# Kernel optimization log

Hardware: AMD Instinct MI355X
Metric: run time of the kernel (lower is better)

Reference implementation:

```python
import jax, jax.numpy as jnp
import numpy as np

G = 4        # split_group
H = 64       # hidden_size_t = 256 // 4 (causal -> //1)
I = 64       # input_size_t  = 256 // 4
EPS = 1e-5


def _lstm(x, W_ih, W_hh, b):
    """Grouped unidirectional LSTM, PyTorch gate order (i,f,g,o).
    x: (G,B,T,I); W_ih: (G,4H,I); W_hh: (G,4H,H); b: (G,4H) -> (G,B,T,H)"""
    g, bsz, t, _ = x.shape
    h_dim = W_hh.shape[-1]
    # precompute input projections for all timesteps
    xp = jnp.einsum('gbti,gki->gbtk', x, W_ih) + b[:, None, None, :]  # (G,B,T,4H)
    xp = jnp.moveaxis(xp, 2, 0)  # (T,G,B,4H)

    def step(carry, xt):
        h, c = carry
        gates = xt + jnp.einsum('gbh,gkh->gbk', h, W_hh)
        i_g, f_g, g_g, o_g = jnp.split(gates, 4, axis=-1)
        i_g = jax.nn.sigmoid(i_g)
        f_g = jax.nn.sigmoid(f_g)
        g_g = jnp.tanh(g_g)
        o_g = jax.nn.sigmoid(o_g)
        c = f_g * c + i_g * g_g
        h = o_g * jnp.tanh(c)
        return (h, c), h

    h0 = jnp.zeros((g, bsz, h_dim), x.dtype)
    _, hs = jax.lax.scan(step, (h0, h0), xp)  # hs: (T,G,B,H)
    return jnp.moveaxis(hs, 0, 2)  # (G,B,T,H)


def _bn(x, gamma, beta):
    """BatchNorm1d (training stats) over (B,T) per feature. x: (B,T,F)"""
    mean = x.mean(axis=(0, 1))
    var = x.var(axis=(0, 1))
    return (x - mean) * jax.lax.rsqrt(var + EPS) * gamma + beta


def setup_inputs() -> dict:
    key = jax.random.key(0)
    ks = jax.random.split(key, 12)
    s = 0.1
    F = G * H
    return {
        'inpt': jax.random.normal(ks[0], (32, 1000, 256), jnp.float32),
        'W_ih1': jax.random.normal(ks[1], (G, 4 * H, I), jnp.float32) * s,
        'W_hh1': jax.random.normal(ks[2], (G, 4 * H, H), jnp.float32) * s,
        'b1': jax.random.normal(ks[3], (G, 4 * H), jnp.float32) * s,
        'W_ih2': jax.random.normal(ks[4], (G, 4 * H, H), jnp.float32) * s,
        'W_hh2': jax.random.normal(ks[5], (G, 4 * H, H), jnp.float32) * s,
        'b2': jax.random.normal(ks[6], (G, 4 * H), jnp.float32) * s,
        'gamma1': jnp.ones((F,), jnp.float32) + jax.random.normal(ks[7], (F,)) * 0.01,
        'beta1': jax.random.normal(ks[8], (F,), jnp.float32) * 0.01,
        'gamma2': jnp.ones((F,), jnp.float32) + jax.random.normal(ks[9], (F,)) * 0.01,
        'beta2': jax.random.normal(ks[10], (F,), jnp.float32) * 0.01,
    }


def reference(inpt, W_ih1, W_hh1, b1, W_ih2, W_hh2, b2, gamma1, beta1, gamma2, beta2):
    B, T, F = inpt.shape
    # chunk along features -> (G,B,T,I)
    xg = jnp.transpose(inpt.reshape(B, T, G, I), (2, 0, 1, 3))
    y1 = _lstm(xg, W_ih1, W_hh1, b1)  # (G,B,T,H)
    # torch.stack(dim=-1) + flatten: feature index = h*G + g (interleaved)
    x = jnp.transpose(y1, (1, 2, 3, 0)).reshape(B, T, H * G)
    x = _bn(x, gamma1, beta1)
    # chunk again into G contiguous groups of size H
    xg2 = jnp.transpose(x.reshape(B, T, G, H), (2, 0, 1, 3))
    y2 = _lstm(xg2, W_ih2, W_hh2, b2)  # (G,B,T,H)
    # torch.cat(dim=-1): contiguous groups
    x = jnp.transpose(y2, (1, 2, 0, 3)).reshape(B, T, G * H)
    x = _bn(x, gamma2, beta2)
    return x
```

## Files before the change

### kernel.cpp

```cpp
#include <hip/hip_runtime.h>
#include <math.h>

#define G 4
#define H 64
#define T 1000
#define B 32
#define ROWS (B*T)
#define SS 8

typedef _Float16 f16;
typedef _Float16 f16x2 __attribute__((ext_vector_type(2)));

#if defined(__has_builtin)
#if __has_builtin(__builtin_amdgcn_fdot2)
#define HAVE_FDOT2 1
#endif
#endif

__device__ __forceinline__ float dot2(f16x2 a, f16x2 b, float c) {
#ifdef HAVE_FDOT2
    return __builtin_amdgcn_fdot2(a, b, c, false);
#else
    return fmaf((float)a[0], (float)b[0], fmaf((float)a[1], (float)b[1], c));
#endif
}

__device__ __forceinline__ float sigm(float x) {
    return 1.f / (1.f + __expf(-x));
}
__device__ __forceinline__ float tanh_f(float x) {
    return 2.f / (1.f + __expf(-2.f * x)) - 1.f;
}

typedef const __attribute__((address_space(1))) void gas_void;
typedef __attribute__((address_space(3))) void las_void;

template<int LAYER>
__device__ void rec_wave4(const float* __restrict__ xp,
                          const float* __restrict__ Whh,
                          float* __restrict__ out,
                          float* __restrict__ stateh, float* __restrict__ statec,
                          float* __restrict__ sums,
                          int t0, int t1, int tcmax)
{
    __builtin_amdgcn_s_setprio(1);
    __shared__ __align__(16) float xbuf[2][SS][4][256];
    __shared__ __align__(16) _Float16 hx[4][64];
    const int wv = threadIdx.x >> 6;
    const int c  = threadIdx.x & 63;
    const int sq = blockIdx.x * 4 + wv;
    const int g = sq >> 5, b = sq & 31;

    f16x2 wpk[4][32];
    #pragma unroll
    for (int gt = 0; gt < 4; ++gt) {
        const float2* wp = (const float2*)&Whh[(size_t)((g * 256 + gt * 64 + c) << 6)];
        #pragma unroll
        for (int k = 0; k < 32; ++k) {
            float2 v = wp[k];
            f16x2 r; r[0] = (f16)v.x; r[1] = (f16)v.y;
            wpk[gt][k] = r;
        }
    }

    f16x2 hpk[32];
    float cst;
    if (t0 == 0) {
        #pragma unroll
        for (int k = 0; k < 32; ++k) { f16x2 z; z[0] = (f16)0.f; z[1] = (f16)0.f; hpk[k] = z; }
        cst = 0.f;
    } else {
        const float2* sh = (const float2*)&stateh[sq * 64];
        #pragma unroll
        for (int k = 0; k < 32; ++k) {
            float2 v = sh[k];
            f16x2 r; r[0] = (f16)v.x; r[1] = (f16)v.y;
            hpk[k] = r;
        }
        cst = statec[sq * 64 + c];
    }

    const float* xpb = xp + (size_t)sq * tcmax * 256;

    #pragma unroll
    for (int j = 0; j < SS; ++j) {
        const float* gsrc = xpb + (size_t)j * 256 + c * 4;
        __builtin_amdgcn_global_load_lds((gas_void*)gsrc,
                                         (las_void*)&xbuf[0][j][wv][0], 16, 0, 0);
    }
    asm volatile("s_waitcnt vmcnt(0)" ::: "memory");
    __builtin_amdgcn_sched_barrier(0);

    float st_s = 0.f, st_ss = 0.f, hl = 0.f;
    const int ngrp = (t1 - t0) / SS;
    for (int grp = 0; grp < ngrp; ++grp) {
        const int cur = grp & 1;
        if (grp + 1 < ngrp) {
            const int lbase = (grp + 1) * SS;
            #pragma unroll
            for (int j = 0; j < SS; ++j) {
                const float* gsrc = xpb + (size_t)(lbase + j) * 256 + c * 4;
                __builtin_amdgcn_global_load_lds((gas_void*)gsrc,
                                                 (las_void*)&xbuf[cur ^ 1][j][wv][0],
                                                 16, 0, 0);
            }
        }
        #pragma unroll
        for (int j = 0; j < SS; ++j) {
            float4 pj = *(const float4*)&xbuf[cur][j][wv][c * 4];
            float pre[4];
            {
                float a0 = 0.f, a1 = 0.f;
                #pragma unroll
                for (int k = 0; k < 32; k += 2) {
                    a0 = dot2(wpk[0][k],     hpk[k],     a0);
                    a1 = dot2(wpk[0][k + 1], hpk[k + 1], a1);
                }
                pre[0] = (a0 + a1) + pj.x;
            }
            {
                float a0 = 0.f, a1 = 0.f;
                #pragma unroll
                for (int k = 0; k < 32; k += 2) {
                    a0 = dot2(wpk[1][k],     hpk[k],     a0);
                    a1 = dot2(wpk[1][k + 1], hpk[k + 1], a1);
                }
                pre[1] = (a0 + a1) + pj.y;
            }
            {
                float a0 = 0.f, a1 = 0.f;
                #pragma unroll
                for (int k = 0; k < 32; k += 2) {
                    a0 = dot2(wpk[2][k],     hpk[k],     a0);
                    a1 = dot2(wpk[2][k + 1], hpk[k + 1], a1);
                }
                pre[2] = (a0 + a1) + pj.z;
            }
            {
                float a0 = 0.f, a1 = 0.f;
                #pragma unroll
                for (int k = 0; k < 32; k += 2) {
                    a0 = dot2(wpk[3][k],     hpk[k],     a0);
                    a1 = dot2(wpk[3][k + 1], hpk[k + 1], a1);
                }
                pre[3] = (a0 + a1) + pj.w;
            }
            float ig = sigm(pre[0]);
            float fg = sigm(pre[1]);
            float gg = tanh_f(pre[2]);
            float og = sigm(pre[3]);
            cst = fmaf(fg, cst, ig * gg);
            float h = og * tanh_f(cst);
            int t = t0 + grp * SS + j;
            if (LAYER == 1) out[((size_t)b * T + t) * 256 + c * 4 + g] = h;
            else            out[((size_t)b * T + t) * 256 + g * 64 + c] = h;
            st_s += h;
            st_ss = fmaf(h, h, st_ss);
            hl = h;
            hx[wv][c] = (f16)h;
            const float4* hp = (const float4*)&hx[wv][0];
            #pragma unroll
            for (int q = 0; q < 8; ++q) {
                float4 v = hp[q];
                hpk[q * 4 + 0] = __builtin_bit_cast(f16x2, v.x);
                hpk[q * 4 + 1] = __builtin_bit_cast(f16x2, v.y);
                hpk[q * 4 + 2] = __builtin_bit_cast(f16x2, v.z);
                hpk[q * 4 + 3] = __builtin_bit_cast(f16x2, v.w);
            }
        }
        asm volatile("s_waitcnt vmcnt(8)" ::: "memory");
        __builtin_amdgcn_sched_barrier(0);
    }
    stateh[sq * 64 + c] = hl;
    statec[sq * 64 + c] = cst;
    int f = (LAYER == 1) ? (c * 4 + g) : (g * 64 + c);
    atomicAdd(&sums[f], st_s);
    atomicAdd(&sums[256 + f], st_ss);
}

template<bool BN>
__device__ void proj_tile(int id,
                          const float* __restrict__ xin,
                          const float* __restrict__ Wih,
                          const float* __restrict__ bias,
                          const float* __restrict__ ac,
                          float* __restrict__ xp,
                          int t0, int tcn, int tcmax, int TT)
{
    __shared__ __align__(16) float xs[64][68];
    __shared__ __align__(16) float wsm[64][68];

    const int tt = id % TT; id /= TT;
    const int b = id & 31;
    const int g = id >> 5;
    const int tid = threadIdx.x;
    const int tx = tid & 15, ty = tid >> 4;

    #pragma unroll
    for (int j = 0; j < 4; ++j) {
        int idx = j * 1024 + tid * 4;
        int r = idx >> 6, ci = idx & 63;
        int tg = t0 + tt * 64 + r; if (tg > T - 1) tg = T - 1;
        float4 v = *(const float4*)&xin[((size_t)b * T + tg) * 256 + g * 64 + ci];
        if (BN) {
            float4 a4 = *(const float4*)&ac[g * 64 + ci];
            float4 c4 = *(const float4*)&ac[256 + g * 64 + ci];
            v.x = fmaf(v.x, a4.x, c4.x);
            v.y = fmaf(v.y, a4.y, c4.y);
            v.z = fmaf(v.z, a4.z, c4.z);
            v.w = fmaf(v.w, a4.w, c4.w);
        }
        *(float4*)&xs[r][ci] = v;
    }

    float* xpb = xp + (size_t)(g * 32 + b) * tcmax * 256;

    for (int kt = 0; kt < 4; ++kt) {
        __syncthreads();
        #pragma unroll
        for (int j = 0; j < 4; ++j) {
            int idx = j * 1024 + tid * 4;
            int r = idx >> 6, ci = idx & 63;
            float4 v = *(const float4*)&Wih[(size_t)((g * 256 + kt * 64 + r) << 6) + ci];
            *(float4*)&wsm[r][ci] = v;
        }
        __syncthreads();

        float acc[4][4] = {};
        #pragma unroll
        for (int i4 = 0; i4 < 16; ++i4) {
            float4 xv[4], wv[4];
            #pragma unroll
            for (int q = 0; q < 4; ++q) xv[q] = *(const float4*)&xs[ty * 4 + q][i4 * 4];
            #pragma unroll
            for (int q = 0; q < 4; ++q) wv[q] = *(const float4*)&wsm[tx + 16 * q][i4 * 4];
            #pragma unroll
            for (int a = 0; a < 4; ++a)
                #pragma unroll
                for (int q = 0; q < 4; ++q) {
                    acc[a][q] = fmaf(xv[a].x, wv[q].x, acc[a][q]);
                    acc[a][q] = fmaf(xv[a].y, wv[q].y, acc[a][q]);
                    acc[a][q] = fmaf(xv[a].z, wv[q].z, acc[a][q]);
                    acc[a][q] = fmaf(xv[a].w, wv[q].w, acc[a][q]);
                }
        }

        float bq[4];
        #pragma unroll
        for (int q = 0; q < 4; ++q) bq[q] = bias[g * 256 + kt * 64 + tx + 16 * q];
        #pragma unroll
        for (int a = 0; a < 4; ++a) {
            int tloc = tt * 64 + ty * 4 + a;
            if (tloc < tcn) {
                #pragma unroll
                for (int q = 0; q < 4; ++q)
                    xpb[(size_t)tloc * 256 + (tx + 16 * q) * 4 + kt] = acc[a][q] + bq[q];
            }
        }
    }
}

template<int LAYER, bool PBN>
__global__ __launch_bounds__(256, 1)
void fused3(const float* __restrict__ xpA, const float* __restrict__ Whh,
            float* __restrict__ out,
            float* __restrict__ stateh, float* __restrict__ statec,
            float* __restrict__ sums,
            int t0, int t1, int tcmax,
            const float* __restrict__ xin, const float* __restrict__ Wih,
            const float* __restrict__ bias, const float* __restrict__ acbn,
            float* __restrict__ xpB, int t0n, int tcnn, int TTn)
{
    if (blockIdx.x < 32) {
        rec_wave4<LAYER>(xpA, Whh, out, stateh, statec, sums, t0, t1, tcmax);
    } else {
        proj_tile<PBN>(blockIdx.x - 32, xin, Wih, bias, acbn, xpB,
                       t0n, tcnn, tcmax, TTn);
    }
}

template<bool BN>
__global__ __launch_bounds__(256)
void xp_proj(const float* __restrict__ xin, const float* __restrict__ Wih,
             const float* __restrict__ bias, const float* __restrict__ ac,
             float* __restrict__ xp, int t0, int tcn, int tcmax, int TT)
{
    proj_tile<BN>(blockIdx.x, xin, Wih, bias, ac, xp, t0, tcn, tcmax, TT);
}

template<int LAYER>
__global__ __launch_bounds__(256, 1)
void rec_kernel(const float* __restrict__ xin,
                const float* __restrict__ Wih,
                const float* __restrict__ Whh,
                const float* __restrict__ bias,
                const float* __restrict__ bnac,
                float* __restrict__ out)
{
    const int g = blockIdx.x & 3;
    const int b = blockIdx.x >> 2;
    const int k = threadIdx.x;

    __shared__ __align__(16) float xsh[2][64];
    __shared__ __align__(16) float hsh[64];
    __shared__ __align__(16) float gsh[256];

    float wih[64], whh[64];
    {
        const float4* wi = (const float4*)(Wih + (size_t)(g * 256 + k) * 64);
        const float4* wh = (const float4*)(Whh + (size_t)(g * 256 + k) * 64);
        #pragma unroll
        for (int i = 0; i < 16; ++i) {
            float4 v = wi[i];
            wih[4*i] = v.x; wih[4*i+1] = v.y; wih[4*i+2] = v.z; wih[4*i+3] = v.w;
            float4 u = wh[i];
            whh[4*i] = u.x; whh[4*i+1] = u.y; whh[4*i+2] = u.z; whh[4*i+3] = u.w;
        }
    }
    const float bk = bias[g * 256 + k];
    const long rowbase = (long)b * T;
    const int  colbase = g * 64;

    float c = 0.f, af = 1.f, cf = 0.f;
    float xa = 0.f, xb = 0.f;

    if (k < 64) {
        if (LAYER == 2) { af = bnac[colbase + k]; cf = bnac[256 + colbase + k]; }
        hsh[k] = 0.f;
        float x0 = xin[(rowbase + 0) * 256 + colbase + k];
        xsh[0][k] = (LAYER == 2) ? fmaf(x0, af, cf) : x0;
        xa = xin[(rowbase + 1) * 256 + colbase + k];
        xb = xin[(rowbase + 2) * 256 + colbase + k];
    }
    __syncthreads();

    for (int t = 0; t < T; ++t) {
        const int cur = t & 1;
        float xn = 0.f;
        if (k < 64) {
            int tp = t + 3; if (tp > T - 1) tp = T - 1;
            xn = xin[(rowbase + tp) * 256 + colbase + k];
        }
        const float* xs = xsh[cur];
        float a0 = 0.f, a1 = 0.f, a2 = 0.f, a3 = 0.f;
        #pragma unroll
        for (int i = 0; i < 64; i += 4) {
            a0 = fmaf(wih[i],     xs[i],     a0);
            a1 = fmaf(wih[i + 1], xs[i + 1], a1);
            a2 = fmaf(wih[i + 2], xs[i + 2], a2);
            a3 = fmaf(wih[i + 3], xs[i + 3], a3);
        }
        #pragma unroll
        for (int jq = 0; jq < 64; jq += 4) {
            a0 = fmaf(whh[jq],     hsh[jq],     a0);
            a1 = fmaf(whh[jq + 1], hsh[jq + 1], a1);
            a2 = fmaf(whh[jq + 2], hsh[jq + 2], a2);
            a3 = fmaf(whh[jq + 3], hsh[jq + 3], a3);
        }
        const float acc = bk + ((a0 + a1) + (a2 + a3));
        const float act = (k >= 128 && k < 192) ? tanh_f(acc) : sigm(acc);
        gsh[k] = act;
        __syncthreads();

        if (k < 64) {
            const float ig = gsh[k];
            const float fg = gsh[64 + k];
            const float gg = gsh[128 + k];
            const float og = gsh[192 + k];
            c = fmaf(fg, c, ig * gg);
            const float h = og * tanh_f(c);
            hsh[k] = h;
            const long rrow = rowbase + t;
            if (LAYER == 1) out[rrow * 256 + k * 4 + g] = h;
            else            out[rrow * 256 + colbase + k] = h;
            xsh[cur ^ 1][k] = fmaf(xa, af, cf);
            xa = xb; xb = xn;
        }
        __syncthreads();
    }
}

__global__ void zero_ws(float* sums, int n) {
    int i = blockIdx.x * blockDim.x + threadIdx.x;
    if (i < n) sums[i] = 0.f;
}

__global__ __launch_bounds__(256) void stats_reduce(const float* __restrict__ x,
                                                    float* __restrict__ sums)
{
    float s = 0.f, ss = 0.f;
    for (int r = blockIdx.x; r < ROWS; r += gridDim.x) {
        float v = x[(long)r * 256 + threadIdx.x];
        s += v;
        ss = fmaf(v, v, ss);
    }
    atomicAdd(&sums[threadIdx.x], s);
    atomicAdd(&sums[256 + threadIdx.x], ss);
}

__global__ void stats_finalize(const float* __restrict__ sums,
                               const float* __restrict__ gamma,
                               const float* __restrict__ beta,
                               float* __restrict__ ac)
{
    int f = threadIdx.x;
    const float invN = 1.f / (float)ROWS;
    float mean = sums[f] * invN;
    float var  = fmaf(-mean, mean, sums[256 + f] * invN);
    float a = gamma[f] * rsqrtf(var + 1e-5f);
    ac[f]       = a;
    ac[256 + f] = fmaf(-mean, a, beta[f]);
}

__global__ __launch_bounds__(256) void bn_apply(float* __restrict__ x,
                                                const float* __restrict__ ac)
{
    __shared__ float a_s[256], c_s[256];
    a_s[threadIdx.x] = ac[threadIdx.x];
    c_s[threadIdx.x] = ac[256 + threadIdx.x];
    __syncthreads();
    const long n4 = (long)ROWS * 64;
    for (long i = (long)blockIdx.x * blockDim.x + threadIdx.x; i < n4;
         i += (long)gridDim.x * blockDim.x) {
        float4 v = ((float4*)x)[i];
        int f0 = (int)((i * 4) & 255);
        v.x = fmaf(v.x, a_s[f0],     c_s[f0]);
        v.y = fmaf(v.y, a_s[f0 + 1], c_s[f0 + 1]);
        v.z = fmaf(v.z, a_s[f0 + 2], c_s[f0 + 2]);
        v.w = fmaf(v.w, a_s[f0 + 3], c_s[f0 + 3]);
        ((float4*)x)[i] = v;
    }
}

extern "C" void kernel_launch(void* const* d_in, const int* in_sizes, int n_in,
                              void* d_out, int out_size, void* d_ws, size_t ws_size,
                              hipStream_t stream)
{
    const float* inpt   = (const float*)d_in[0];
    const float* Wih1   = (const float*)d_in[1];
    const float* Whh1   = (const float*)d_in[2];
    const float* b1     = (const float*)d_in[3];
    const float* Wih2   = (const float*)d_in[4];
    const float* Whh2   = (const float*)d_in[5];
    const float* b2     = (const float*)d_in[6];
    const float* gamma1 = (const float*)d_in[7];
    const float* beta1  = (const float*)d_in[8];
    const float* gamma2 = (const float*)d_in[9];
    const float* beta2  = (const float*)d_in[10];
    float* out  = (float*)d_out;

    float* sums1 = (float*)d_ws;
    float* sums2 = sums1 + 512;
    float* acbn1 = sums2 + 512;
    float* acbn2 = acbn1 + 512;
    float* sth   = acbn2 + 512;
    float* stc   = sth + 8192;
    float* xpb   = stc + 8192;

    const size_t fixedB = (size_t)(4 * 512 + 2 * 8192) * 4;
    const long perT = 128L * 256L * 4L;
    long availPair = ((long)ws_size - (long)fixedB) / (2L * perT);

    int chunks[8]; int nch = 0;
    if (availPair >= 440) {
        chunks[0] = 32; chunks[1] = 80; chunks[2] = 200;
        chunks[3] = 440; chunks[4] = 248; nch = 5;
    } else if (availPair >= SS) {
        int Tc = (int)(availPair & ~(long)(SS - 1));
        int acc = 0;
        while (acc < T && nch < 8) {
            int c = T - acc; if (c > Tc) c = Tc;
            chunks[nch++] = c; acc += c;
        }
        if (acc < T) nch = 0;
    }

    if (nch > 0) {
        int tcmax = 0;
        for (int i = 0; i < nch; ++i) if (chunks[i] > tcmax) tcmax = chunks[i];
        float* buf[2] = { xpb, xpb + (size_t)tcmax * 128 * 256 };
        zero_ws<<<4, 256, 0, stream>>>(sums1, 1024);

        for (int layer = 1; layer <= 2; ++layer) {
            const float* xin  = (layer == 1) ? inpt : out;
            const float* Wih  = (layer == 1) ? Wih1 : Wih2;
            const float* Whh  = (layer == 1) ? Whh1 : Whh2;
            const float* bb   = (layer == 1) ? b1 : b2;
            float* sums       = (layer == 1) ? sums1 : sums2;

            int t0 = 0;
            int TT0 = (chunks[0] + 63) / 64;
            if (layer == 1)
                xp_proj<false><<<128 * TT0, 256, 0, stream>>>(
                    xin, Wih, bb, nullptr, buf[0], 0, chunks[0], tcmax, TT0);
            else
                xp_proj<true><<<128 * TT0, 256, 0, stream>>>(
                    xin, Wih, bb, acbn1, buf[0], 0, chunks[0], tcmax, TT0);

            for (int c = 0; c < nch; ++c) {
                int t1 = t0 + chunks[c];
                int t0n = t1;
                int tcnn = (c + 1 < nch) ? chunks[c + 1] : 0;
                int TTn = (tcnn + 63) / 64;
                int grid = 32 + 128 * TTn;
                if (layer == 1)
                    fused3<1, false><<<grid, 256, 0, stream>>>(
                        buf[c & 1], Whh, out, sth, stc, sums, t0, t1, tcmax,
                        xin, Wih, bb, nullptr, buf[(c + 1) & 1], t0n, tcnn, TTn);
                else
                    fused3<2, true><<<grid, 256, 0, stream>>>(
                        buf[c & 1], Whh, out, sth, stc, sums, t0, t1, tcmax,
                        xin, Wih, bb, acbn1, buf[(c + 1) & 1], t0n, tcnn, TTn);
                t0 = t1;
            }
            if (layer == 1)
                stats_finalize<<<1, 256, 0, stream>>>(sums1, gamma1, beta1, acbn1);
            else
                stats_finalize<<<1, 256, 0, stream>>>(sums2, gamma2, beta2, acbn2);
        }
        bn_apply<<<2048, 256, 0, stream>>>(out, acbn2);
    } else {
        zero_ws<<<2, 256, 0, stream>>>(sums1, 512);
        rec_kernel<1><<<G * B, 256, 0, stream>>>(inpt, Wih1, Whh1, b1, nullptr, out);
        stats_reduce<<<256, 256, 0, stream>>>(out, sums1);
        stats_finalize<<<1, 256, 0, stream>>>(sums1, gamma1, beta1, acbn1);
        rec_kernel<2><<<G * B, 256, 0, stream>>>(out, Wih2, Whh2, b2, acbn1, out);
        zero_ws<<<2, 256, 0, stream>>>(sums2, 512);
        stats_reduce<<<256, 256, 0, stream>>>(out, sums2);
        stats_finalize<<<1, 256, 0, stream>>>(sums2, gamma2, beta2, acbn2);
        bn_apply<<<2048, 256, 0, stream>>>(out, acbn2);
    }
}
```

Before: 1.492 ms.

## Alias recurrence and projection shared memory, halve prefetch depth, rebalance time chunks

The recurrence and projection code paths of the fused kernel now share one shared-memory buffer instead of holding separate static arrays. The xp prefetch group size drops from 8 to 4 steps, which shrinks the LDS double-buffer and requires a matching vmcnt wait. The time-chunk schedule changes from five chunks to three (128, 440, 432), cutting the number of launches and pipeline stages. The smaller per-block LDS footprint may let projection blocks co-reside better. The trade-off is more frequent wait points in the recurrence loop and a longer initial chunk that is not overlapped with projection work.

Result: slower. 2.590 ms (+73.5%).

```diff
diff --git a/kernel.cpp b/kernel.cpp
--- a/kernel.cpp
+++ b/kernel.cpp
@@ -6,7 +6,13 @@
 #define T 1000
 #define B 32
 #define ROWS (B*T)
-#define SS 8
+#define SS 4
+
+#define SM_XBUF   0
+#define SM_HX     32768
+#define SM_XS     0
+#define SM_WSM    17408
+#define SM_BYTES  34816
 
 typedef _Float16 f16;
 typedef _Float16 f16x2 __attribute__((ext_vector_type(2)));
@@ -36,7 +42,8 @@
 typedef __attribute__((address_space(3))) void las_void;
 
 template<int LAYER>
-__device__ void rec_wave4(const float* __restrict__ xp,
+__device__ void rec_wave4(char* smem,
+                          const float* __restrict__ xp,
                           const float* __restrict__ Whh,
                           float* __restrict__ out,
                           float* __restrict__ stateh, float* __restrict__ statec,
@@ -44,8 +51,8 @@
                           int t0, int t1, int tcmax)
 {
     __builtin_amdgcn_s_setprio(1);
-    __shared__ __align__(16) float xbuf[2][SS][4][256];
-    __shared__ __align__(16) _Float16 hx[4][64];
+    float*     xbuf = (float*)(smem + SM_XBUF);
+    _Float16*  hx   = (_Float16*)(smem + SM_HX);
     const int wv = threadIdx.x >> 6;
     const int c  = threadIdx.x & 63;
     const int sq = blockIdx.x * 4 + wv;
@@ -86,7 +93,8 @@
     for (int j = 0; j < SS; ++j) {
         const float* gsrc = xpb + (size_t)j * 256 + c * 4;
         __builtin_amdgcn_global_load_lds((gas_void*)gsrc,
-                                         (las_void*)&xbuf[0][j][wv][0], 16, 0, 0);
+                                         (las_void*)&xbuf[(j * 4 + wv) * 256],
+                                         16, 0, 0);
     }
     asm volatile("s_waitcnt vmcnt(0)" ::: "memory");
     __builtin_amdgcn_sched_barrier(0);
@@ -100,14 +108,15 @@
             #pragma unroll
             for (int j = 0; j < SS; ++j) {
                 const float* gsrc = xpb + (size_t)(lbase + j) * 256 + c * 4;
-                __builtin_amdgcn_global_load_lds((gas_void*)gsrc,
-                                                 (las_void*)&xbuf[cur ^ 1][j][wv][0],
-                                                 16, 0, 0);
+                __builtin_amdgcn_global_load_lds(
+                    (gas_void*)gsrc,
+                    (las_void*)&xbuf[(((cur ^ 1) * SS + j) * 4 + wv) * 256],
+                    16, 0, 0);
             }
         }
         #pragma unroll
         for (int j = 0; j < SS; ++j) {
-            float4 pj = *(const float4*)&xbuf[cur][j][wv][c * 4];
+            float4 pj = *(const float4*)&xbuf[((cur * SS + j) * 4 + wv) * 256 + c * 4];
             float pre[4];
             {
                 float a0 = 0.f, a1 = 0.f;
@@ -157,8 +166,8 @@
             st_s += h;
             st_ss = fmaf(h, h, st_ss);
             hl = h;
-            hx[wv][c] = (f16)h;
-            const float4* hp = (const float4*)&hx[wv][0];
+            hx[wv * 64 + c] = (f16)h;
+            const float4* hp = (const float4*)&hx[wv * 64];
             #pragma unroll
             for (int q = 0; q < 8; ++q) {
                 float4 v = hp[q];
@@ -168,7 +177,7 @@
                 hpk[q * 4 + 3] = __builtin_bit_cast(f16x2, v.w);
             }
         }
-        asm volatile("s_waitcnt vmcnt(8)" ::: "memory");
+        asm volatile("s_waitcnt vmcnt(4)" ::: "memory");
         __builtin_amdgcn_sched_barrier(0);
     }
     stateh[sq * 64 + c] = hl;
@@ -179,7 +188,7 @@
 }
 
 template<bool BN>
-__device__ void proj_tile(int id,
+__device__ void proj_tile(char* smem, int id,
                           const float* __restrict__ xin,
                           const float* __restrict__ Wih,
                           const float* __restrict__ bias,
@@ -187,8 +196,9 @@
                           float* __restrict__ xp,
                           int t0, int tcn, int tcmax, int TT)
 {
-    __shared__ __align__(16) float xs[64][68];
-    __shared__ __align__(16) float wsm[64][68];
+    typedef float row68[68];
+    row68* xs  = (row68*)(smem + SM_XS);
+    row68* wsm = (row68*)(smem + SM_WSM);
 
     const int tt = id % TT; id /= TT;
     const int b = id & 31;
@@ -271,10 +281,11 @@
             const float* __restrict__ bias, const float* __restrict__ acbn,
             float* __restrict__ xpB, int t0n, int tcnn, int TTn)
 {
+    __shared__ __align__(16) char smem[SM_BYTES];
     if (blockIdx.x < 32) {
-        rec_wave4<LAYER>(xpA, Whh, out, stateh, statec, sums, t0, t1, tcmax);
+        rec_wave4<LAYER>(smem, xpA, Whh, out, stateh, statec, sums, t0, t1, tcmax);
     } else {
-        proj_tile<PBN>(blockIdx.x - 32, xin, Wih, bias, acbn, xpB,
+        proj_tile<PBN>(smem, blockIdx.x - 32, xin, Wih, bias, acbn, xpB,
                        t0n, tcnn, tcmax, TTn);
     }
 }
@@ -285,7 +296,8 @@
              const float* __restrict__ bias, const float* __restrict__ ac,
              float* __restrict__ xp, int t0, int tcn, int tcmax, int TT)
 {
-    proj_tile<BN>(blockIdx.x, xin, Wih, bias, ac, xp, t0, tcn, tcmax, TT);
+    __shared__ __align__(16) char smem[SM_BYTES];
+    proj_tile<BN>(smem, blockIdx.x, xin, Wih, bias, ac, xp, t0, tcn, tcmax, TT);
 }
 
 template<int LAYER>
@@ -463,8 +475,7 @@
 
     int chunks[8]; int nch = 0;
     if (availPair >= 440) {
-        chunks[0] = 32; chunks[1] = 80; chunks[2] = 200;
-        chunks[3] = 440; chunks[4] = 248; nch = 5;
+        chunks[0] = 128; chunks[1] = 440; chunks[2] = 432; nch = 3;
     } else if (availPair >= SS) {
         int Tc = (int)(availPair & ~(long)(SS - 1));
         int acc = 0;
```
